# Optimization experiments

Hardware: AMD Instinct MI355X
Metric: run time of the kernel (lower is better)

## Reference

```python
import jax, jax.numpy as jnp
import numpy as np

B, T, N, D = 16, 12, 10000, 2
E = 320000


def setup_inputs() -> dict:
    key = jax.random.key(0)
    k1, k2, k3 = jax.random.split(key, 3)
    predictions = jax.random.normal(k1, (B, T, N, D), dtype=jnp.float32)
    targets = jax.random.normal(k2, (B, T, N, D), dtype=jnp.float32)
    edge_index = jax.random.randint(k3, (2, E), 0, N, dtype=jnp.int64)
    return {"predictions": predictions, "targets": targets, "edge_index": edge_index}


def reference(predictions, targets, edge_index):
    # weights from __init__ defaults
    mse_w, spatial_w, temporal_w, conservation_w = 1.0, 0.1, 0.05, 0.02

    # main loss: MAE (use_mae=True)
    main_loss = jnp.mean(jnp.abs(predictions - targets))

    # spatial consistency: the per-(b,t) python loop of mse over edges,
    # averaged over batch*pred_len, equals one global mean over [B,T,E,D]
    src, dst = edge_index[0], edge_index[1]
    pred_diff = jnp.abs(predictions[:, :, src] - predictions[:, :, dst])  # [B,T,E,D]
    targ_diff = jnp.abs(targets[:, :, src] - targets[:, :, dst])
    spatial_loss = jnp.mean((pred_diff - targ_diff) ** 2)

    # temporal smoothness: first-order time differences
    pd_t = predictions[:, 1:] - predictions[:, :-1]
    td_t = targets[:, 1:] - targets[:, :-1]
    temporal_loss = jnp.mean((pd_t - td_t) ** 2)

    # conservation: sum over nodes
    pred_sum = predictions.sum(axis=2)  # [B,T,D]
    targ_sum = targets.sum(axis=2)
    conservation_loss = jnp.mean((pred_sum - targ_sum) ** 2)

    total_loss = (mse_w * main_loss + spatial_w * spatial_loss
                  + temporal_w * temporal_loss + conservation_w * conservation_loss)

    # order: loss, main_loss, spatial_loss, temporal_loss, conservation_loss
    return jnp.stack([total_loss, main_loss, spatial_loss, temporal_loss, conservation_loss])
```

## Files before the change

kernel.cpp:

```cpp
#include <hip/hip_runtime.h>
#include <hip/hip_fp16.h>

#define BB 16
#define TT 12
#define NN 10000
#define DD 2
#define EE 320000
#define BT 192
#define TOT 3840000
#define SLICE 20000

#define NCH 96
#define SLICES 16
#define EPS 20000
#define SPATB (NCH*SLICES)
#define SPATG (SPATB + BT)

#define PACKB 942
#define EOFFB 1250
#define PREPG (PACKB + EOFFB)

#define EOFF_BOFF 32768
#define W2_BOFF   1314816
#define NEED (W2_BOFF + (size_t)NCH * NN * 2 * 4)

typedef float v2f __attribute__((ext_vector_type(2)));

__device__ __forceinline__ __half2 pkh2(float a, float b) {
    auto t = __builtin_amdgcn_cvt_pkrtz(a, b);
    return *reinterpret_cast<__half2*>(&t);
}
__device__ __forceinline__ void slot_acc(unsigned a, unsigned b, __half2& acc) {
    v2f ap = __builtin_amdgcn_cvt_pk_f32_fp8((int)a, false);
    v2f at = __builtin_amdgcn_cvt_pk_f32_fp8((int)a, true);
    v2f bp = __builtin_amdgcn_cvt_pk_f32_fp8((int)b, false);
    v2f bq = __builtin_amdgcn_cvt_pk_f32_fp8((int)b, true);
    __half2 d = __hsub2(__habs2(__hsub2(pkh2(ap[0], ap[1]), pkh2(bp[0], bp[1]))),
                        __habs2(__hsub2(pkh2(at[0], at[1]), pkh2(bq[0], bq[1]))));
    acc = __hfma2(d, d, acc);
}

__global__ __launch_bounds__(256) void prep_kernel(const float* __restrict__ p,
                                                   const float* __restrict__ tg,
                                                   const int* __restrict__ idx,
                                                   char* __restrict__ wsb) {
    int g = blockIdx.x;
    if (g < PACKB) {
        __shared__ unsigned tile[64][33];
        int ng = g / 6, cg = g % 6;
        int n0 = ng * 64;
        int ln = threadIdx.x & 63, r = threadIdx.x >> 6;
        int n = n0 + ln;
        if (n < NN) {
            for (int sl = r; sl < 32; sl += 4) {
                int bt = cg * 32 + sl;
                size_t e = (size_t)bt * SLICE + (size_t)n * 2;
                float2 pv = *reinterpret_cast<const float2*>(p + e);
                float2 tv = *reinterpret_cast<const float2*>(tg + e);
                int pk = __builtin_amdgcn_cvt_pk_fp8_f32(pv.x, pv.y, 0, false);
                pk = __builtin_amdgcn_cvt_pk_fp8_f32(tv.x, tv.y, pk, true);
                tile[ln][sl] = (unsigned)pk;
            }
        }
        __syncthreads();
        unsigned* w2c = (unsigned*)(wsb + W2_BOFF);
        for (int f = threadIdx.x; f < 2048; f += 256) {
            int c2 = f >> 7, j2 = f & 127;
            int nn2 = j2 >> 1, k2 = j2 & 1;
            int n2 = n0 + nn2;
            if (n2 < NN) {
                int c = cg * 16 + c2;
                w2c[((unsigned)(c * NN + n2) << 1) + k2] = tile[nn2][c2 * 2 + k2];
            }
        }
    } else {
        int e = (g - PACKB) * 256 + threadIdx.x;
        if (e < EE) {
            unsigned* eoff = (unsigned*)(wsb + EOFF_BOFF);
            eoff[e] = (unsigned)idx[e] | ((unsigned)idx[EE + e] << 16);
        }
    }
}

__global__ __launch_bounds__(1024, 8) void spatial_kernel(const uint2* __restrict__ w2c2,
                                                          const unsigned* __restrict__ eoff,
                                                          const float* __restrict__ p,
                                                          const float* __restrict__ tg,
                                                          float* __restrict__ ws) {
    __shared__ uint2 nd[NN];
    __shared__ float red[64];
    int bid = blockIdx.x;
    int tid = threadIdx.x;

    if (bid >= SPATB) {
        int bt = bid - SPATB;
        size_t base = (size_t)bt * SLICE;
        bool inner = (bt % TT) < TT - 1;
        const float2* p2  = (const float2*)(p + base);
        const float2* t2  = (const float2*)(tg + base);
        const float2* pn2 = (const float2*)(p + base + SLICE);
        const float2* tn2 = (const float2*)(tg + base + SLICE);
        float m = 0.f, w = 0.f, cx = 0.f, cy = 0.f;
        for (int j = tid; j < NN; j += 1024) {
            float2 pv = p2[j], tv = t2[j];
            m += fabsf(pv.x - tv.x) + fabsf(pv.y - tv.y);
            cx += pv.x - tv.x;
            cy += pv.y - tv.y;
            if (inner) {
                float2 pn = pn2[j], tn = tn2[j];
                float d0 = (pn.x - pv.x) - (tn.x - tv.x);
                float d1 = (pn.y - pv.y) - (tn.y - tv.y);
                w = fmaf(d0, d0, w);
                w = fmaf(d1, d1, w);
            }
        }
        for (int o = 32; o; o >>= 1) {
            m += __shfl_xor(m, o); w += __shfl_xor(w, o);
            cx += __shfl_xor(cx, o); cy += __shfl_xor(cy, o);
        }
        int wid = tid >> 6;
        if ((tid & 63) == 0) {
            red[wid] = m; red[16 + wid] = w; red[32 + wid] = cx; red[48 + wid] = cy;
        }
        __syncthreads();
        if (tid == 0) {
            float M = 0, W = 0, CX = 0, CY = 0;
            for (int k = 0; k < 16; ++k) {
                M += red[k]; W += red[16 + k]; CX += red[32 + k]; CY += red[48 + k];
            }
            ws[bt] = M;
            ws[1536 + bt] = W;
            ws[3072 + 2 * bt] = CX;
            ws[3072 + 2 * bt + 1] = CY;
        }
        return;
    }

    int c = bid % NCH;
    int s = bid / NCH;
    const uint4* src4 = (const uint4*)(w2c2 + (size_t)c * NN);
    uint4* nd4 = (uint4*)nd;
    for (int i = tid; i < NN / 2; i += 1024)
        nd4[i] = src4[i];
    __syncthreads();

    int e = s * EPS + tid;
    const int eend = s * EPS + EPS;
    __half2 acc0 = __float2half2_rn(0.f), acc1 = __float2half2_rn(0.f);
    while (e + 1024 < eend) {
        unsigned eo1 = eoff[e], eo2 = eoff[e + 1024];
        uint2 A1 = nd[eo1 & 0xFFFFu], B1 = nd[eo1 >> 16];
        uint2 A2 = nd[eo2 & 0xFFFFu], B2 = nd[eo2 >> 16];
        slot_acc(A1.x, B1.x, acc0);
        slot_acc(A1.y, B1.y, acc1);
        slot_acc(A2.x, B2.x, acc0);
        slot_acc(A2.y, B2.y, acc1);
        e += 2048;
    }
    if (e < eend) {
        unsigned eo = eoff[e];
        uint2 A = nd[eo & 0xFFFFu], B = nd[eo >> 16];
        slot_acc(A.x, B.x, acc0);
        slot_acc(A.y, B.y, acc1);
    }
    float acc = __low2float(acc0) + __high2float(acc0)
              + __low2float(acc1) + __high2float(acc1);
    for (int o = 32; o; o >>= 1) acc += __shfl_xor(acc, o);
    if ((tid & 63) == 0) red[tid >> 6] = acc;
    __syncthreads();
    if (tid == 0) {
        float t = 0.f;
        for (int k = 0; k < 16; ++k) t += red[k];
        ws[6144 + bid] = t;
    }
}

__global__ __launch_bounds__(1024) void finalize_kernel(const float* __restrict__ ws,
                                                        float* __restrict__ out) {
    int tid = threadIdx.x;
    float a = 0, bv = 0, sp = 0, cq = 0;
    if (tid < BT) { a = ws[tid]; bv = ws[1536 + tid]; }
    for (int k = tid; k < SPATB; k += 1024) sp += ws[6144 + k];
    if (tid < BT * DD) { float cs = ws[3072 + tid]; cq = cs * cs; }
    for (int o = 32; o; o >>= 1) {
        a += __shfl_xor(a, o); bv += __shfl_xor(bv, o);
        sp += __shfl_xor(sp, o); cq += __shfl_xor(cq, o);
    }
    __shared__ float ra[16], rb[16], rs[16], rc[16];
    int wid = tid >> 6;
    if ((tid & 63) == 0) { ra[wid] = a; rb[wid] = bv; rs[wid] = sp; rc[wid] = cq; }
    __syncthreads();
    if (tid == 0) {
        float A = 0, B2 = 0, S = 0, C = 0;
        for (int k = 0; k < 16; k++) { A += ra[k]; B2 += rb[k]; S += rs[k]; C += rc[k]; }
        float mainl = A / (float)TOT;
        float temp  = B2 / (float)(BB * (TT - 1) * NN * DD);
        float spat  = S / ((float)BT * (float)EE * (float)DD);
        float cons  = C / (float)(BT * DD);
        out[0] = mainl + 0.1f * spat + 0.05f * temp + 0.02f * cons;
        out[1] = mainl; out[2] = spat; out[3] = temp; out[4] = cons;
    }
}

__global__ __launch_bounds__(256) void stream_fb(const float* __restrict__ p,
                                                 const float* __restrict__ tg,
                                                 float* __restrict__ ws) {
    int b = blockIdx.x;
    int bt = b >> 3, part = b & 7;
    int tt = bt % TT;
    size_t base = (size_t)bt * SLICE;
    bool inner = (tt < TT - 1);
    float m = 0.f, w = 0.f, c = 0.f;
    int j0 = part * 2500;
    for (int j = j0 + threadIdx.x; j < j0 + 2500; j += 256) {
        size_t jj = base + j;
        float pv = p[jj], tv = tg[jj];
        m += fabsf(pv - tv);
        c += pv - tv;
        if (inner) {
            float pn = p[jj + SLICE], tn = tg[jj + SLICE];
            float dd = (pn - pv) - (tn - tv);
            w += dd * dd;
        }
    }
    for (int o = 32; o >= 2; o >>= 1) {
        m += __shfl_xor(m, o); w += __shfl_xor(w, o); c += __shfl_xor(c, o);
    }
    m += __shfl_xor(m, 1);
    w += __shfl_xor(w, 1);
    __shared__ float sm[4], sw[4], s0[4], s1[4];
    int wid = threadIdx.x >> 6, lane = threadIdx.x & 63;
    if (lane == 0) { sm[wid] = m; sw[wid] = w; s0[wid] = c; }
    if (lane == 1) { s1[wid] = c; }
    __syncthreads();
    if (threadIdx.x == 0) {
        float a = 0, bv = 0, c0 = 0, c1 = 0;
        for (int k = 0; k < 4; k++) { a += sm[k]; bv += sw[k]; c0 += s0[k]; c1 += s1[k]; }
        ws[b] = a; ws[1536 + b] = bv;
        ws[3072 + 2 * b] = c0; ws[3072 + 2 * b + 1] = c1;
    }
}

__global__ __launch_bounds__(256) void spatial_fb(const float* __restrict__ p,
                                                  const float* __restrict__ tg,
                                                  const int* __restrict__ idx,
                                                  float* __restrict__ ws) {
    int lane = threadIdx.x & 63;
    int wave = (blockIdx.x * 256 + threadIdx.x) >> 6;
    float s = 0.f;
    for (int e = wave; e < EE; e += SPATB * 4) {
        int sn = idx[e] * DD, dn = idx[EE + e] * DD;
        for (int bt = lane; bt < BT; bt += 64) {
            size_t base = (size_t)bt * SLICE;
            float2 ps = *reinterpret_cast<const float2*>(p + base + sn);
            float2 pd = *reinterpret_cast<const float2*>(p + base + dn);
            float2 ts = *reinterpret_cast<const float2*>(tg + base + sn);
            float2 td = *reinterpret_cast<const float2*>(tg + base + dn);
            float d0 = fabsf(ps.x - pd.x) - fabsf(ts.x - td.x);
            float d1 = fabsf(ps.y - pd.y) - fabsf(ts.y - td.y);
            s = fmaf(d0, d0, s);
            s = fmaf(d1, d1, s);
        }
    }
    for (int o = 32; o; o >>= 1) s += __shfl_xor(s, o);
    __shared__ float sv[4];
    if (lane == 0) sv[threadIdx.x >> 6] = s;
    __syncthreads();
    if (threadIdx.x == 0) ws[6144 + blockIdx.x] = sv[0] + sv[1] + sv[2] + sv[3];
}

__global__ __launch_bounds__(1024) void finalize_fb(const float* __restrict__ ws,
                                                    float* __restrict__ out) {
    int tid = threadIdx.x;
    float a = 0, bv = 0, sp = 0, cq = 0;
    for (int k = tid; k < 1536; k += 1024) { a += ws[k]; bv += ws[1536 + k]; }
    for (int k = tid; k < SPATB; k += 1024) sp += ws[6144 + k];
    if (tid < BT * DD) {
        int bt = tid >> 1, par = tid & 1;
        float cs = 0;
        for (int part = 0; part < 8; ++part)
            cs += ws[3072 + ((bt * 8 + part) << 1) + par];
        cq = cs * cs;
    }
    for (int o = 32; o; o >>= 1) {
        a += __shfl_xor(a, o); bv += __shfl_xor(bv, o);
        sp += __shfl_xor(sp, o); cq += __shfl_xor(cq, o);
    }
    __shared__ float ra[16], rb[16], rs[16], rc[16];
    int wid = tid >> 6;
    if ((tid & 63) == 0) { ra[wid] = a; rb[wid] = bv; rs[wid] = sp; rc[wid] = cq; }
    __syncthreads();
    if (tid == 0) {
        float A = 0, B2 = 0, S = 0, C = 0;
        for (int k = 0; k < 16; k++) { A += ra[k]; B2 += rb[k]; S += rs[k]; C += rc[k]; }
        float mainl = A / (float)TOT;
        float temp  = B2 / (float)(BB * (TT - 1) * NN * DD);
        float spat  = S / ((float)BT * (float)EE * (float)DD);
        float cons  = C / (float)(BT * DD);
        out[0] = mainl + 0.1f * spat + 0.05f * temp + 0.02f * cons;
        out[1] = mainl; out[2] = spat; out[3] = temp; out[4] = cons;
    }
}

extern "C" void kernel_launch(void* const* d_in, const int* in_sizes, int n_in,
                              void* d_out, int out_size, void* d_ws, size_t ws_size,
                              hipStream_t stream) {
    const float* p  = (const float*)d_in[0];
    const float* tg = (const float*)d_in[1];
    const int*   ix = (const int*)d_in[2];
    float* out = (float*)d_out;
    char*  wsb = (char*)d_ws;
    float* ws  = (float*)d_ws;

    if (ws_size >= NEED) {
        prep_kernel<<<PREPG, 256, 0, stream>>>(p, tg, ix, wsb);
        spatial_kernel<<<SPATG, 1024, 0, stream>>>((const uint2*)(wsb + W2_BOFF),
                                                   (const unsigned*)(wsb + EOFF_BOFF),
                                                   p, tg, ws);
        finalize_kernel<<<1, 1024, 0, stream>>>(ws, out);
    } else {
        stream_fb<<<1536, 256, 0, stream>>>(p, tg, ws);
        spatial_fb<<<SPATB, 256, 0, stream>>>(p, tg, ix, ws);
        finalize_fb<<<1, 1024, 0, stream>>>(ws, out);
    }
}
```

Before: 55.75 us.

## Precompute byte offsets for edge gathers, use fdot2 float accumulation, reorder blocks

Edge indices are now stored as two pre-scaled byte offsets (uint2) rather than a packed 16-bit pair, which removes the mask, shift and scale work in the gather loop at the cost of twice the index bandwidth. The half2 accumulators are replaced by a single float accumulator updated with fdot2, which improves accuracy and cuts instruction count. The streaming (main/temporal/conservation) blocks are moved to the front of the grid so they get scheduled early. The workspace layout is shifted to make room for the larger offset array.

```diff
diff --git a/kernel.cpp b/kernel.cpp
--- a/kernel.cpp
+++ b/kernel.cpp
@@ -21,23 +21,37 @@
 #define PREPG (PACKB + EOFFB)
 
 #define EOFF_BOFF 32768
-#define W2_BOFF   1314816
+#define W2_BOFF   2623488
 #define NEED (W2_BOFF + (size_t)NCH * NN * 2 * 4)
 
 typedef float v2f __attribute__((ext_vector_type(2)));
+typedef _Float16 hv2 __attribute__((ext_vector_type(2)));
+
+#if defined(__has_builtin)
+#if __has_builtin(__builtin_amdgcn_fdot2)
+#define HAVE_FDOT2 1
+#endif
+#endif
 
 __device__ __forceinline__ __half2 pkh2(float a, float b) {
     auto t = __builtin_amdgcn_cvt_pkrtz(a, b);
     return *reinterpret_cast<__half2*>(&t);
 }
-__device__ __forceinline__ void slot_acc(unsigned a, unsigned b, __half2& acc) {
+__device__ __forceinline__ void slot_acc(unsigned a, unsigned b, float& acc) {
     v2f ap = __builtin_amdgcn_cvt_pk_f32_fp8((int)a, false);
     v2f at = __builtin_amdgcn_cvt_pk_f32_fp8((int)a, true);
     v2f bp = __builtin_amdgcn_cvt_pk_f32_fp8((int)b, false);
     v2f bq = __builtin_amdgcn_cvt_pk_f32_fp8((int)b, true);
     __half2 d = __hsub2(__habs2(__hsub2(pkh2(ap[0], ap[1]), pkh2(bp[0], bp[1]))),
                         __habs2(__hsub2(pkh2(at[0], at[1]), pkh2(bq[0], bq[1]))));
-    acc = __hfma2(d, d, acc);
+#ifdef HAVE_FDOT2
+    hv2 dr = *reinterpret_cast<hv2*>(&d);
+    acc = __builtin_amdgcn_fdot2(dr, dr, acc, false);
+#else
+    float2 f = __half22float2(d);
+    acc = fmaf(f.x, f.x, acc);
+    acc = fmaf(f.y, f.y, acc);
+#endif
 }
 
 __global__ __launch_bounds__(256) void prep_kernel(const float* __restrict__ p,
@@ -76,14 +90,15 @@
     } else {
         int e = (g - PACKB) * 256 + threadIdx.x;
         if (e < EE) {
-            unsigned* eoff = (unsigned*)(wsb + EOFF_BOFF);
-            eoff[e] = (unsigned)idx[e] | ((unsigned)idx[EE + e] << 16);
+            uint2* eoff = (uint2*)(wsb + EOFF_BOFF);
+            eoff[e] = make_uint2((unsigned)idx[e] * 8u,
+                                 (unsigned)idx[EE + e] * 8u);
         }
     }
 }
 
 __global__ __launch_bounds__(1024, 8) void spatial_kernel(const uint2* __restrict__ w2c2,
-                                                          const unsigned* __restrict__ eoff,
+                                                          const uint2* __restrict__ eoff,
                                                           const float* __restrict__ p,
                                                           const float* __restrict__ tg,
                                                           float* __restrict__ ws) {
@@ -92,8 +107,8 @@
     int bid = blockIdx.x;
     int tid = threadIdx.x;
 
-    if (bid >= SPATB) {
-        int bt = bid - SPATB;
+    if (bid < BT) {
+        int bt = bid;
         size_t base = (size_t)bt * SLICE;
         bool inner = (bt % TT) < TT - 1;
         const float2* p2  = (const float2*)(p + base);
@@ -136,42 +151,45 @@
         return;
     }
 
-    int c = bid % NCH;
-    int s = bid / NCH;
+    int gb = bid - BT;
+    int c = gb % NCH;
+    int s = gb / NCH;
     const uint4* src4 = (const uint4*)(w2c2 + (size_t)c * NN);
     uint4* nd4 = (uint4*)nd;
     for (int i = tid; i < NN / 2; i += 1024)
         nd4[i] = src4[i];
     __syncthreads();
 
+    const char* ndb = (const char*)nd;
     int e = s * EPS + tid;
     const int eend = s * EPS + EPS;
-    __half2 acc0 = __float2half2_rn(0.f), acc1 = __float2half2_rn(0.f);
+    float acc = 0.f;
     while (e + 1024 < eend) {
-        unsigned eo1 = eoff[e], eo2 = eoff[e + 1024];
-        uint2 A1 = nd[eo1 & 0xFFFFu], B1 = nd[eo1 >> 16];
-        uint2 A2 = nd[eo2 & 0xFFFFu], B2 = nd[eo2 >> 16];
-        slot_acc(A1.x, B1.x, acc0);
-        slot_acc(A1.y, B1.y, acc1);
-        slot_acc(A2.x, B2.x, acc0);
-        slot_acc(A2.y, B2.y, acc1);
+        uint2 o1 = eoff[e], o2 = eoff[e + 1024];
+        uint2 A1 = *(const uint2*)(ndb + o1.x);
+        uint2 B1 = *(const uint2*)(ndb + o1.y);
+        uint2 A2 = *(const uint2*)(ndb + o2.x);
+        uint2 B2 = *(const uint2*)(ndb + o2.y);
+        slot_acc(A1.x, B1.x, acc);
+        slot_acc(A1.y, B1.y, acc);
+        slot_acc(A2.x, B2.x, acc);
+        slot_acc(A2.y, B2.y, acc);
         e += 2048;
     }
     if (e < eend) {
-        unsigned eo = eoff[e];
-        uint2 A = nd[eo & 0xFFFFu], B = nd[eo >> 16];
-        slot_acc(A.x, B.x, acc0);
-        slot_acc(A.y, B.y, acc1);
-    }
-    float acc = __low2float(acc0) + __high2float(acc0)
-              + __low2float(acc1) + __high2float(acc1);
+        uint2 o = eoff[e];
+        uint2 A = *(const uint2*)(ndb + o.x);
+        uint2 B = *(const uint2*)(ndb + o.y);
+        slot_acc(A.x, B.x, acc);
+        slot_acc(A.y, B.y, acc);
+    }
     for (int o = 32; o; o >>= 1) acc += __shfl_xor(acc, o);
     if ((tid & 63) == 0) red[tid >> 6] = acc;
     __syncthreads();
     if (tid == 0) {
         float t = 0.f;
         for (int k = 0; k < 16; ++k) t += red[k];
-        ws[6144 + bid] = t;
+        ws[6144 + gb] = t;
     }
 }
 
@@ -315,7 +333,7 @@
     if (ws_size >= NEED) {
         prep_kernel<<<PREPG, 256, 0, stream>>>(p, tg, ix, wsb);
         spatial_kernel<<<SPATG, 1024, 0, stream>>>((const uint2*)(wsb + W2_BOFF),
-                                                   (const unsigned*)(wsb + EOFF_BOFF),
+                                                   (const uint2*)(wsb + EOFF_BOFF),
                                                    p, tg, ws);
         finalize_kernel<<<1, 1024, 0, stream>>>(ws, out);
     } else {
```

Measured after the change: 55.43 us. Within noise of the previous version (-0.6%).
